# Optimization experiments

Measured on AMD Instinct MI355X. Metric: run time of the kernel, lower is better.

## Reference

```python
import jax, jax.numpy as jnp
import numpy as np

T, H, F, E, K = 2048, 1024, 2816, 8, 2


def setup_inputs() -> dict:
    key = jax.random.key(0)
    k1, k2, k3, k4, k5 = jax.random.split(key, 5)
    hidden_states = jax.random.normal(k1, (T, H), dtype=jnp.float32)
    topk_weights = jax.random.uniform(k2, (T, K), dtype=jnp.float32)
    topk_ids = jax.random.randint(k3, (T, K), 0, E, dtype=jnp.int64)
    gate_up_weights = jax.random.normal(k4, (E, 2 * F, H), dtype=jnp.float32) * 0.02
    down_weights = jax.random.normal(k5, (E, H, F), dtype=jnp.float32) * 0.02
    return {
        'hidden_states': hidden_states,
        'topk_weights': topk_weights,
        'topk_ids': topk_ids,
        'gate_up_weights': gate_up_weights,
        'down_weights': down_weights,
    }


def reference(hidden_states, topk_weights, topk_ids, gate_up_weights, down_weights):
    # Per-token combine weight for each expert: w[e, t] = sum_k topk_w[t,k] * (topk_ids[t,k] == e)
    onehot = jax.nn.one_hot(topk_ids, E, dtype=hidden_states.dtype)       # [T, K, E]
    combine_w = jnp.einsum('tk,tke->et', topk_weights, onehot)            # [E, T]

    # Grouped gate/up GEMM (expressed as batched GEMM over experts)
    gu = jnp.einsum('th,efh->etf', hidden_states, gate_up_weights)        # [E, T, 2F]
    gate, up = gu[..., :F], gu[..., F:]
    act = jax.nn.silu(gate) * up                                          # [E, T, F]

    # Down projection and weighted combine
    y = jnp.einsum('etf,ehf->eth', act, down_weights)                     # [E, T, H]
    out = jnp.einsum('et,eth->th', combine_w, y)                          # [T, H]
    return out
```

## Files before the change

### kernel.cpp

```cpp
#include <hip/hip_runtime.h>
#include <hip/hip_bf16.h>

#define T_TOK 2048
#define H_DIM 1024
#define F_DIM 2816
#define E_NUM 8
#define K_TOP 2
#define NPAIR (T_TOK * K_TOP)

#define BM 128
#define BN 128
#define BK 32
#define KS 56
#define MAXTILES 40

typedef __bf16 bf16_t;
typedef bf16_t bf16x8 __attribute__((ext_vector_type(8)));
typedef float f32x4 __attribute__((ext_vector_type(4)));

#define META_TILEE   16
#define META_TILEROW 64
#define META_TILEEND 112
#define META_S2P     160
#define ACT_OFFSET   65536

__global__ void moe_route(const int* __restrict__ ids, int* __restrict__ meta) {
    __shared__ int cnt[E_NUM], cur[E_NUM];
    const int tid = threadIdx.x;
    if (tid < E_NUM) cnt[tid] = 0;
    __syncthreads();
    for (int p = tid; p < NPAIR; p += blockDim.x)
        atomicAdd(&cnt[ids[p]], 1);
    __syncthreads();
    if (tid == 0) {
        int acc = 0, nt = 0;
        for (int e = 0; e < E_NUM; ++e) {
            cur[e] = acc;
            const int c = cnt[e];
            for (int r = 0; r < c; r += BM) {
                meta[META_TILEE + nt]   = e;
                meta[META_TILEROW + nt] = acc + r;
                meta[META_TILEEND + nt] = acc + c;
                ++nt;
            }
            acc += c;
        }
        meta[0] = nt;
    }
    __syncthreads();
    int* s2p = meta + META_S2P;
    for (int p = tid; p < NPAIR; p += blockDim.x) {
        const int e = ids[p];
        const int s = atomicAdd(&cur[e], 1);
        s2p[s] = p;
    }
}

__device__ inline bf16x8 zero8() {
    bf16x8 v;
#pragma unroll
    for (int j = 0; j < 8; ++j) v[j] = (bf16_t)0.0f;
    return v;
}

__global__ __launch_bounds__(256, 2) void moe_gemm1(
    const float* __restrict__ X, const float* __restrict__ Wgu,
    const int* __restrict__ meta, bf16_t* __restrict__ act)
{
    const int mt = blockIdx.x;
    if (mt >= meta[0]) return;
    const int nt   = blockIdx.y;
    const int e    = meta[META_TILEE + mt];
    const int row0 = meta[META_TILEROW + mt];
    const int rend = meta[META_TILEEND + mt];
    const int* s2p = meta + META_S2P;

    const float* Wg = Wgu + (size_t)e * (2 * F_DIM) * H_DIM + (size_t)nt * BN * H_DIM;
    const float* Wu = Wg + (size_t)F_DIM * H_DIM;

    __shared__ bf16_t As[BM][KS];
    __shared__ bf16_t Bgs[BN][KS];
    __shared__ bf16_t Bus[BN][KS];

    const int tid  = threadIdx.x;
    const int lane = tid & 63;
    const int wid  = tid >> 6;
    const int wm   = (wid >> 1) * 64;
    const int wn   = (wid & 1) * 64;
    const int fr   = lane & 15;
    const int fk   = (lane >> 4) * 8;

    const int koff = (tid & 3) * 8;
    const int rowu[2] = { tid >> 2, 64 + (tid >> 2) };
    const float* aptr[2]; const float* gptr[2]; const float* uptr[2];
    bool aval[2];
    bf16_t* awr[2]; bf16_t* gwr[2]; bf16_t* uwr[2];
#pragma unroll
    for (int s = 0; s < 2; ++s) {
        const int r = rowu[s];
        const int slot = row0 + r;
        aval[s] = (slot < rend);
        const int t = aval[s] ? (s2p[slot] >> 1) : 0;
        aptr[s] = X + (size_t)t * H_DIM + koff;
        gptr[s] = Wg + (size_t)r * H_DIM + koff;
        uptr[s] = Wu + (size_t)r * H_DIM + koff;
        awr[s] = &As[r][koff];
        gwr[s] = &Bgs[r][koff];
        uwr[s] = &Bus[r][koff];
    }

    f32x4 accg[4][4];
    f32x4 accu[4][4];
    const f32x4 zf = {0.0f, 0.0f, 0.0f, 0.0f};
#pragma unroll
    for (int m = 0; m < 4; ++m)
#pragma unroll
        for (int n = 0; n < 4; ++n) { accg[m][n] = zf; accu[m][n] = zf; }

    for (int kk = 0; kk < H_DIM / BK; ++kk) {
        __syncthreads();
        const int go = kk * BK;
#pragma unroll
        for (int s = 0; s < 2; ++s) {
            f32x4 a0 = zf, a1 = zf;
            if (aval[s]) {
                a0 = *(const f32x4*)(aptr[s] + go);
                a1 = *(const f32x4*)(aptr[s] + go + 4);
            }
            const f32x4 g0 = *(const f32x4*)(gptr[s] + go);
            const f32x4 g1 = *(const f32x4*)(gptr[s] + go + 4);
            const f32x4 u0 = *(const f32x4*)(uptr[s] + go);
            const f32x4 u1 = *(const f32x4*)(uptr[s] + go + 4);
            bf16x8 av, gv, uv;
#pragma unroll
            for (int j = 0; j < 4; ++j) {
                av[j] = (bf16_t)a0[j]; av[j + 4] = (bf16_t)a1[j];
                gv[j] = (bf16_t)g0[j]; gv[j + 4] = (bf16_t)g1[j];
                uv[j] = (bf16_t)u0[j]; uv[j + 4] = (bf16_t)u1[j];
            }
            *(bf16x8*)awr[s] = av;
            *(bf16x8*)gwr[s] = gv;
            *(bf16x8*)uwr[s] = uv;
        }
        __syncthreads();

        bf16x8 af[4];
#pragma unroll
        for (int m = 0; m < 4; ++m)
            af[m] = *(const bf16x8*)&As[wm + m * 16 + fr][fk];
#pragma unroll
        for (int n = 0; n < 4; ++n) {
            const bf16x8 gf = *(const bf16x8*)&Bgs[wn + n * 16 + fr][fk];
            const bf16x8 uf = *(const bf16x8*)&Bus[wn + n * 16 + fr][fk];
#pragma unroll
            for (int m = 0; m < 4; ++m) {
                accg[m][n] = __builtin_amdgcn_mfma_f32_16x16x32_bf16(af[m], gf, accg[m][n], 0, 0, 0);
                accu[m][n] = __builtin_amdgcn_mfma_f32_16x16x32_bf16(af[m], uf, accu[m][n], 0, 0, 0);
            }
        }
    }

    const int qrow = (lane >> 4) * 4;
#pragma unroll
    for (int m = 0; m < 4; ++m) {
#pragma unroll
        for (int q = 0; q < 4; ++q) {
            const int r = wm + m * 16 + qrow + q;
            const int slot = row0 + r;
            if (slot < rend) {
                bf16_t* arow = act + (size_t)slot * F_DIM + nt * BN + wn;
#pragma unroll
                for (int n = 0; n < 4; ++n) {
                    const float g = accg[m][n][q];
                    const float u = accu[m][n][q];
                    const float sg = 1.0f / (1.0f + __expf(-g));
                    arow[n * 16 + fr] = (bf16_t)(g * sg * u);
                }
            }
        }
    }
}

__global__ __launch_bounds__(256, 2) void moe_gemm2(
    const bf16_t* __restrict__ act, const float* __restrict__ Wd,
    const float* __restrict__ tkw, const int* __restrict__ meta,
    float* __restrict__ out)
{
    const int mt = blockIdx.x;
    if (mt >= meta[0]) return;
    const int nt   = blockIdx.y;
    const int e    = meta[META_TILEE + mt];
    const int row0 = meta[META_TILEROW + mt];
    const int rend = meta[META_TILEEND + mt];
    const int* s2p = meta + META_S2P;

    const float* Wb = Wd + (size_t)e * H_DIM * F_DIM + (size_t)nt * BN * F_DIM;

    __shared__ bf16_t As[BM][KS];
    __shared__ bf16_t Bs[BN][KS];

    const int tid  = threadIdx.x;
    const int lane = tid & 63;
    const int wid  = tid >> 6;
    const int wm   = (wid >> 1) * 64;
    const int wn   = (wid & 1) * 64;
    const int fr   = lane & 15;
    const int fk   = (lane >> 4) * 8;

    const int koff = (tid & 3) * 8;
    const int rowu[2] = { tid >> 2, 64 + (tid >> 2) };
    const bf16_t* aptr[2]; const float* bptr[2];
    bool aval[2];
    bf16_t* awr[2]; bf16_t* bwr[2];
#pragma unroll
    for (int s = 0; s < 2; ++s) {
        const int r = rowu[s];
        const int slot = row0 + r;
        aval[s] = (slot < rend);
        aptr[s] = act + (size_t)(aval[s] ? slot : 0) * F_DIM + koff;
        bptr[s] = Wb + (size_t)r * F_DIM + koff;
        awr[s] = &As[r][koff];
        bwr[s] = &Bs[r][koff];
    }

    f32x4 acc[4][4];
    const f32x4 zf = {0.0f, 0.0f, 0.0f, 0.0f};
#pragma unroll
    for (int m = 0; m < 4; ++m)
#pragma unroll
        for (int n = 0; n < 4; ++n) acc[m][n] = zf;

    for (int kk = 0; kk < F_DIM / BK; ++kk) {
        __syncthreads();
        const int go = kk * BK;
#pragma unroll
        for (int s = 0; s < 2; ++s) {
            bf16x8 av = zero8();
            if (aval[s]) av = *(const bf16x8*)(aptr[s] + go);
            const f32x4 b0 = *(const f32x4*)(bptr[s] + go);
            const f32x4 b1 = *(const f32x4*)(bptr[s] + go + 4);
            bf16x8 bv;
#pragma unroll
            for (int j = 0; j < 4; ++j) {
                bv[j] = (bf16_t)b0[j]; bv[j + 4] = (bf16_t)b1[j];
            }
            *(bf16x8*)awr[s] = av;
            *(bf16x8*)bwr[s] = bv;
        }
        __syncthreads();

        bf16x8 af[4];
#pragma unroll
        for (int m = 0; m < 4; ++m)
            af[m] = *(const bf16x8*)&As[wm + m * 16 + fr][fk];
#pragma unroll
        for (int n = 0; n < 4; ++n) {
            const bf16x8 bf = *(const bf16x8*)&Bs[wn + n * 16 + fr][fk];
#pragma unroll
            for (int m = 0; m < 4; ++m)
                acc[m][n] = __builtin_amdgcn_mfma_f32_16x16x32_bf16(af[m], bf, acc[m][n], 0, 0, 0);
        }
    }

    const int qrow = (lane >> 4) * 4;
#pragma unroll
    for (int m = 0; m < 4; ++m) {
#pragma unroll
        for (int q = 0; q < 4; ++q) {
            const int r = wm + m * 16 + qrow + q;
            const int slot = row0 + r;
            if (slot < rend) {
                const int p = s2p[slot];
                const int t = p >> 1;
                const float w = tkw[p];
                float* orow = out + (size_t)t * H_DIM + nt * BN + wn;
#pragma unroll
                for (int n = 0; n < 4; ++n)
                    atomicAdd(&orow[n * 16 + fr], w * acc[m][n][q]);
            }
        }
    }
}

extern "C" void kernel_launch(void* const* d_in, const int* in_sizes, int n_in,
                              void* d_out, int out_size, void* d_ws, size_t ws_size,
                              hipStream_t stream) {
    const float* X   = (const float*)d_in[0];
    const float* tkw = (const float*)d_in[1];
    const int*   ids = (const int*)d_in[2];
    const float* Wgu = (const float*)d_in[3];
    const float* Wd  = (const float*)d_in[4];
    float* out = (float*)d_out;

    int*    meta = (int*)d_ws;
    bf16_t* act  = (bf16_t*)((char*)d_ws + ACT_OFFSET);

    hipMemsetAsync(d_out, 0, (size_t)T_TOK * H_DIM * sizeof(float), stream);
    moe_route<<<1, 256, 0, stream>>>(ids, meta);
    moe_gemm1<<<dim3(MAXTILES, F_DIM / BN), 256, 0, stream>>>(X, Wgu, meta, act);
    moe_gemm2<<<dim3(MAXTILES, H_DIM / BN), 256, 0, stream>>>(act, Wd, tkw, meta, out);
}
```

Baseline: 582.3 us.

## Pre-convert weights to bf16, gather tokens, use direct-to-LDS loads and split-K down GEMM

When the workspace is large enough, separate kernels first convert the gate/up and down weights to bf16 and gather the routed token rows into a contiguous bf16 buffer. New GEMM kernels then load tiles straight into LDS with global_load_lds, use swizzled 1-D block indexing for cache locality, and split the down GEMM's K dimension in two so more blocks run at once. The aim is to halve the bytes the GEMMs read and drop the in-loop fp32-to-bf16 conversion. In exchange, every call pays a full pass over the fp32 weights to convert them, and split-K doubles the atomic adds into the output.

```diff
diff --git a/kernel.cpp b/kernel.cpp
--- a/kernel.cpp
+++ b/kernel.cpp
@@ -13,6 +13,12 @@
 #define BK 32
 #define KS 56
 #define MAXTILES 40
+#define NT1 22
+#define NT2 8
+#define KSPLIT2 2
+#define FS2 (F_DIM / KSPLIT2)
+#define NK1 (H_DIM / BK)
+#define NK2 (FS2 / BK)
 
 typedef __bf16 bf16_t;
 typedef bf16_t bf16x8 __attribute__((ext_vector_type(8)));
@@ -22,7 +28,17 @@
 #define META_TILEROW 64
 #define META_TILEEND 112
 #define META_S2P     160
-#define ACT_OFFSET   65536
+#define ACT_OFFSET   65536ULL
+#define XG_OFFSET    (ACT_OFFSET + 23068672ULL)
+#define WGU_OFFSET   (XG_OFFSET + 8388608ULL)
+#define WD_OFFSET    (WGU_OFFSET + 92274688ULL)
+#define WS_NEED      (WD_OFFSET + 46137344ULL)
+
+__device__ inline void gload_lds16(const void* g, void* l) {
+    __builtin_amdgcn_global_load_lds(
+        (const __attribute__((address_space(1))) void*)g,
+        (__attribute__((address_space(3))) void*)l, 16, 0, 0);
+}
 
 __global__ void moe_route(const int* __restrict__ ids, int* __restrict__ meta) {
     __shared__ int cnt[E_NUM], cur[E_NUM];
@@ -56,6 +72,228 @@
     }
 }
 
+
+__global__ void conv_bf(const float* __restrict__ src, bf16_t* __restrict__ dst, int n8) {
+    for (int i = blockIdx.x * blockDim.x + threadIdx.x; i < n8; i += gridDim.x * blockDim.x) {
+        const f32x4 a = *(const f32x4*)(src + (size_t)i * 8);
+        const f32x4 b = *(const f32x4*)(src + (size_t)i * 8 + 4);
+        bf16x8 v;
+#pragma unroll
+        for (int j = 0; j < 4; ++j) { v[j] = (bf16_t)a[j]; v[j + 4] = (bf16_t)b[j]; }
+        *(bf16x8*)(dst + (size_t)i * 8) = v;
+    }
+}
+
+__global__ void gather_x(const float* __restrict__ X, const int* __restrict__ meta,
+                         bf16_t* __restrict__ xg) {
+    const int slot = blockIdx.x;
+    const int t = meta[META_S2P + slot] >> 1;
+    const float* src = X + (size_t)t * H_DIM + threadIdx.x * 8;
+    bf16_t* dst = xg + (size_t)slot * H_DIM + threadIdx.x * 8;
+    const f32x4 a = *(const f32x4*)src;
+    const f32x4 b = *(const f32x4*)(src + 4);
+    bf16x8 v;
+#pragma unroll
+    for (int j = 0; j < 4; ++j) { v[j] = (bf16_t)a[j]; v[j + 4] = (bf16_t)b[j]; }
+    *(bf16x8*)dst = v;
+}
+
+__global__ __launch_bounds__(256, 2) void moe_gemm1_bf(
+    const bf16_t* __restrict__ Xg, const bf16_t* __restrict__ Wgu,
+    const int* __restrict__ meta, bf16_t* __restrict__ act)
+{
+    const int h = blockIdx.x;
+    const int L = (h & 7) * (MAXTILES * NT1 / 8) + (h >> 3);
+    const int mt = L % MAXTILES;
+    const int nt = L / MAXTILES;
+    if (mt >= meta[0]) return;
+    const int e    = meta[META_TILEE + mt];
+    const int row0 = meta[META_TILEROW + mt];
+    const int rend = meta[META_TILEEND + mt];
+
+    const bf16_t* Wg = Wgu + (size_t)e * (2 * F_DIM) * H_DIM + (size_t)nt * BN * H_DIM;
+    const bf16_t* Wu = Wg + (size_t)F_DIM * H_DIM;
+
+    __shared__ bf16_t As[BM][BK];
+    __shared__ bf16_t Bgs[BN][BK];
+    __shared__ bf16_t Bus[BN][BK];
+
+    const int tid  = threadIdx.x;
+    const int lane = tid & 63;
+    const int w    = tid >> 6;
+    const int wm   = (w >> 1) * 64;
+    const int wn   = (w & 1) * 64;
+    const int fr   = lane & 15;
+    const int fk   = (lane >> 4) * 8;
+
+    const int lr = lane >> 2;
+    const int ce = (lane & 3) * 8;
+    const bf16_t* a_src[2]; const bf16_t* g_src[2]; const bf16_t* u_src[2];
+    bf16_t *a_dst[2], *g_dst[2], *u_dst[2];
+#pragma unroll
+    for (int i = 0; i < 2; ++i) {
+        const int r = i * 64 + w * 16 + lr;
+        a_src[i] = Xg + (size_t)(row0 + r) * H_DIM + ce;
+        g_src[i] = Wg + (size_t)r * H_DIM + ce;
+        u_src[i] = Wu + (size_t)r * H_DIM + ce;
+        const int lb = (i * 4 + w) * 512;
+        a_dst[i] = &As[0][0] + lb;
+        g_dst[i] = &Bgs[0][0] + lb;
+        u_dst[i] = &Bus[0][0] + lb;
+    }
+
+    f32x4 accg[4][4];
+    f32x4 accu[4][4];
+    const f32x4 zf = {0.0f, 0.0f, 0.0f, 0.0f};
+#pragma unroll
+    for (int m = 0; m < 4; ++m)
+#pragma unroll
+        for (int n = 0; n < 4; ++n) { accg[m][n] = zf; accu[m][n] = zf; }
+
+    for (int kk = 0; kk < NK1; ++kk) {
+        const int go = kk * BK;
+#pragma unroll
+        for (int i = 0; i < 2; ++i) {
+            gload_lds16(a_src[i] + go, a_dst[i]);
+            gload_lds16(g_src[i] + go, g_dst[i]);
+            gload_lds16(u_src[i] + go, u_dst[i]);
+        }
+        __syncthreads();
+
+        bf16x8 af[4];
+#pragma unroll
+        for (int m = 0; m < 4; ++m)
+            af[m] = *(const bf16x8*)&As[wm + m * 16 + fr][fk];
+#pragma unroll
+        for (int n = 0; n < 4; ++n) {
+            const bf16x8 gf = *(const bf16x8*)&Bgs[wn + n * 16 + fr][fk];
+            const bf16x8 uf = *(const bf16x8*)&Bus[wn + n * 16 + fr][fk];
+#pragma unroll
+            for (int m = 0; m < 4; ++m) {
+                accg[m][n] = __builtin_amdgcn_mfma_f32_16x16x32_bf16(af[m], gf, accg[m][n], 0, 0, 0);
+                accu[m][n] = __builtin_amdgcn_mfma_f32_16x16x32_bf16(af[m], uf, accu[m][n], 0, 0, 0);
+            }
+        }
+        __syncthreads();
+    }
+
+    const int qrow = (lane >> 4) * 4;
+#pragma unroll
+    for (int m = 0; m < 4; ++m) {
+#pragma unroll
+        for (int q = 0; q < 4; ++q) {
+            const int r = wm + m * 16 + qrow + q;
+            const int slot = row0 + r;
+            if (slot < rend) {
+                bf16_t* arow = act + (size_t)slot * F_DIM + nt * BN + wn;
+#pragma unroll
+                for (int n = 0; n < 4; ++n) {
+                    const float g = accg[m][n][q];
+                    const float u = accu[m][n][q];
+                    const float sg = 1.0f / (1.0f + __expf(-g));
+                    arow[n * 16 + fr] = (bf16_t)(g * sg * u);
+                }
+            }
+        }
+    }
+}
+
+__global__ __launch_bounds__(256, 2) void moe_gemm2_bf(
+    const bf16_t* __restrict__ act, const bf16_t* __restrict__ Wd,
+    const float* __restrict__ tkw, const int* __restrict__ meta,
+    float* __restrict__ out)
+{
+    const int h = blockIdx.x;
+    const int L = (h & 7) * (MAXTILES * NT2 * KSPLIT2 / 8) + (h >> 3);
+    const int mt = L % MAXTILES;
+    const int q0 = L / MAXTILES;
+    const int nt = q0 % NT2;
+    const int ks = q0 / NT2;
+    if (mt >= meta[0]) return;
+    const int e    = meta[META_TILEE + mt];
+    const int row0 = meta[META_TILEROW + mt];
+    const int rend = meta[META_TILEEND + mt];
+    const int* s2p = meta + META_S2P;
+
+    const bf16_t* Wb = Wd + (size_t)e * H_DIM * F_DIM + (size_t)nt * BN * F_DIM + ks * FS2;
+    const bf16_t* Ab = act + ks * FS2;
+
+    __shared__ bf16_t As[BM][BK];
+    __shared__ bf16_t Bs[BN][BK];
+
+    const int tid  = threadIdx.x;
+    const int lane = tid & 63;
+    const int w    = tid >> 6;
+    const int wm   = (w >> 1) * 64;
+    const int wn   = (w & 1) * 64;
+    const int fr   = lane & 15;
+    const int fk   = (lane >> 4) * 8;
+
+    const int lr = lane >> 2;
+    const int ce = (lane & 3) * 8;
+    const bf16_t* a_src[2]; const bf16_t* b_src[2];
+    bf16_t *a_dst[2], *b_dst[2];
+#pragma unroll
+    for (int i = 0; i < 2; ++i) {
+        const int r = i * 64 + w * 16 + lr;
+        a_src[i] = Ab + (size_t)(row0 + r) * F_DIM + ce;
+        b_src[i] = Wb + (size_t)r * F_DIM + ce;
+        const int lb = (i * 4 + w) * 512;
+        a_dst[i] = &As[0][0] + lb;
+        b_dst[i] = &Bs[0][0] + lb;
+    }
+
+    f32x4 acc[4][4];
+    const f32x4 zf = {0.0f, 0.0f, 0.0f, 0.0f};
+#pragma unroll
+    for (int m = 0; m < 4; ++m)
+#pragma unroll
+        for (int n = 0; n < 4; ++n) acc[m][n] = zf;
+
+    for (int kk = 0; kk < NK2; ++kk) {
+        const int go = kk * BK;
+#pragma unroll
+        for (int i = 0; i < 2; ++i) {
+            gload_lds16(a_src[i] + go, a_dst[i]);
+            gload_lds16(b_src[i] + go, b_dst[i]);
+        }
+        __syncthreads();
+
+        bf16x8 af[4];
+#pragma unroll
+        for (int m = 0; m < 4; ++m)
+            af[m] = *(const bf16x8*)&As[wm + m * 16 + fr][fk];
+#pragma unroll
+        for (int n = 0; n < 4; ++n) {
+            const bf16x8 bf = *(const bf16x8*)&Bs[wn + n * 16 + fr][fk];
+#pragma unroll
+            for (int m = 0; m < 4; ++m)
+                acc[m][n] = __builtin_amdgcn_mfma_f32_16x16x32_bf16(af[m], bf, acc[m][n], 0, 0, 0);
+        }
+        __syncthreads();
+    }
+
+    const int qrow = (lane >> 4) * 4;
+#pragma unroll
+    for (int m = 0; m < 4; ++m) {
+#pragma unroll
+        for (int q = 0; q < 4; ++q) {
+            const int r = wm + m * 16 + qrow + q;
+            const int slot = row0 + r;
+            if (slot < rend) {
+                const int p = s2p[slot];
+                const int t = p >> 1;
+                const float wgt = tkw[p];
+                float* orow = out + (size_t)t * H_DIM + nt * BN + wn;
+#pragma unroll
+                for (int n = 0; n < 4; ++n)
+                    atomicAdd(&orow[n * 16 + fr], wgt * acc[m][n][q]);
+            }
+        }
+    }
+}
+
+
 __device__ inline bf16x8 zero8() {
     bf16x8 v;
 #pragma unroll
@@ -117,7 +355,7 @@
 #pragma unroll
         for (int n = 0; n < 4; ++n) { accg[m][n] = zf; accu[m][n] = zf; }
 
-    for (int kk = 0; kk < H_DIM / BK; ++kk) {
+    for (int kk = 0; kk < NK1; ++kk) {
         __syncthreads();
         const int go = kk * BK;
 #pragma unroll
@@ -272,11 +510,11 @@
             if (slot < rend) {
                 const int p = s2p[slot];
                 const int t = p >> 1;
-                const float w = tkw[p];
+                const float wgt = tkw[p];
                 float* orow = out + (size_t)t * H_DIM + nt * BN + wn;
 #pragma unroll
                 for (int n = 0; n < 4; ++n)
-                    atomicAdd(&orow[n * 16 + fr], w * acc[m][n][q]);
+                    atomicAdd(&orow[n * 16 + fr], wgt * acc[m][n][q]);
             }
         }
     }
@@ -292,11 +530,23 @@
     const float* Wd  = (const float*)d_in[4];
     float* out = (float*)d_out;
 
-    int*    meta = (int*)d_ws;
-    bf16_t* act  = (bf16_t*)((char*)d_ws + ACT_OFFSET);
+    int*    meta   = (int*)d_ws;
+    bf16_t* act    = (bf16_t*)((char*)d_ws + ACT_OFFSET);
 
     hipMemsetAsync(d_out, 0, (size_t)T_TOK * H_DIM * sizeof(float), stream);
     moe_route<<<1, 256, 0, stream>>>(ids, meta);
-    moe_gemm1<<<dim3(MAXTILES, F_DIM / BN), 256, 0, stream>>>(X, Wgu, meta, act);
-    moe_gemm2<<<dim3(MAXTILES, H_DIM / BN), 256, 0, stream>>>(act, Wd, tkw, meta, out);
-}
+
+    if (ws_size >= WS_NEED) {
+        bf16_t* xg     = (bf16_t*)((char*)d_ws + XG_OFFSET);
+        bf16_t* wgu_bf = (bf16_t*)((char*)d_ws + WGU_OFFSET);
+        bf16_t* wd_bf  = (bf16_t*)((char*)d_ws + WD_OFFSET);
+        conv_bf<<<2048, 256, 0, stream>>>(Wgu, wgu_bf, 5767168);
+        conv_bf<<<2048, 256, 0, stream>>>(Wd, wd_bf, 2883584);
+        gather_x<<<NPAIR, 128, 0, stream>>>(X, meta, xg);
+        moe_gemm1_bf<<<MAXTILES * NT1, 256, 0, stream>>>(xg, wgu_bf, meta, act);
+        moe_gemm2_bf<<<MAXTILES * NT2 * KSPLIT2, 256, 0, stream>>>(act, wd_bf, tkw, meta, out);
+    } else {
+        moe_gemm1<<<dim3(MAXTILES, NT1), 256, 0, stream>>>(X, Wgu, meta, act);
+        moe_gemm2<<<dim3(MAXTILES, NT2), 256, 0, stream>>>(act, Wd, tkw, meta, out);
+    }
+}
```

After: 506.1 us. 13.1% less time.
